# Performance work log

Hardware: AMD Instinct MI355X
Metric: run time of the kernel (lower is better)

## Reference

```python
import jax, jax.numpy as jnp
import numpy as np

# CycleFC1w1a constants (from init_kwargs / gen_offset)
IN_CH = 384
KH, KW = 1, 7  # cycle kernel; actual conv weight is 1x1
START = (KH * KW) // 2  # 3


def _gen_offset_x(C):
    # kernel_size[0] == 1 branch: off_y = 0, off_x[i] = (i + START) % KW - KW // 2
    i = jnp.arange(C)
    return (i + START) % KW - KW // 2  # int32, values in [-3, 3]


def setup_inputs() -> dict:
    key = jax.random.key(0)
    k1, k2, k3 = jax.random.split(key, 3)
    x = jax.random.normal(k1, (64, IN_CH, 32, 32), dtype=jnp.float32)
    weight = jax.random.normal(k2, (IN_CH, IN_CH), dtype=jnp.float32) * 0.05  # [out_ch, in_ch]
    bias = jax.random.normal(k3, (IN_CH,), dtype=jnp.float32) * 0.01
    return {"x": x, "weight": weight, "bias": bias}


def reference(x, weight, bias):
    B, C, H, W = x.shape
    # BinaryQuantizer forward: sign()
    xb = jnp.sign(x)
    wb = jnp.sign(weight)  # [O, C]

    # Fixed per-channel integer horizontal offsets -> exact shifted gather
    off_x = _gen_offset_x(C)                                  # [C]
    cols = jnp.arange(W)[None, :] + off_x[:, None]            # [C, W] sample col = w + off
    valid = (cols >= 0) & (cols < W)                          # zero-pad out of bounds
    cols_c = jnp.clip(cols, 0, W - 1)
    # gather along width per channel: [B, C, H, W]
    g = jnp.take_along_axis(xb, cols_c[None, :, None, :], axis=3)
    g = g * valid[None, :, None, :].astype(x.dtype)

    # pointwise (1x1) channel-mixing conv
    out = jnp.einsum('bchw,oc->bohw', g, wb) + bias[None, :, None, None]
    return out
```

## Files before the change

kernel.cpp:

```cpp
#include <hip/hip_runtime.h>
#include <stdint.h>


#define IN_CH 384
#define HH 32
#define WW 32
#define BB 64
#define HR 4

constexpr uint64_t P7(int t) {
  uint64_t m = 0;
  for (int k = 0; k < 64; ++k)
    if (k % 7 == t) m |= (1ull << k);
  return m;
}
__device__ __constant__ uint64_t Pm[7] = {P7(0), P7(1), P7(2), P7(3), P7(4), P7(5), P7(6)};

__global__ __launch_bounds__(64) void cyc_prep(const float* __restrict__ wgt,
                                               const float* __restrict__ bias,
                                               uint64_t* __restrict__ wbg,
                                               float* __restrict__ bias2t) {
  const int o = blockIdx.x;
  const int lane = threadIdx.x;
  __shared__ uint64_t wb_sh[6];
#pragma unroll
  for (int j = 0; j < 6; ++j) {
    uint64_t m = __ballot(wgt[o * IN_CH + j * 64 + lane] < 0.0f);
    if (lane == 0) wb_sh[j] = m;
  }
  __syncthreads();
  if (lane < 6) wbg[o * 6 + lane] = wb_sh[lane];
  if (lane < WW) {
    const int w = lane;
    int nv = 0, corr = 0;
#pragma unroll
    for (int j = 0; j < 6; ++j) {
      uint64_t V = 0;
#pragma unroll
      for (int d = -3; d <= 3; ++d) {
        int wd = w + d;
        if (wd >= 0 && wd < WW) V |= Pm[(d - j + 14) % 7];
      }
      nv += __popcll(V);
      corr += __popcll(wb_sh[j] & ~V);
    }
    bias2t[w * IN_CH + o] = bias[o] + (float)nv + 2.0f * (float)corr;
  }
}

__global__ __launch_bounds__(768) void cyc_main(const float* __restrict__ x,
                                                const uint64_t* __restrict__ wbg,
                                                const float* __restrict__ bias2t,
                                                float* __restrict__ out) {
  __shared__ uint64_t sh_X[HR][WW][6];
  __shared__ uint64_t sh_G[HR][WW][6];
  const int t = threadIdx.x;
  const int b = blockIdx.x >> 3;
  const int h0 = (blockIdx.x & 7) * HR;
  const int wave = t >> 6, lane = t & 63;

#pragma unroll
  for (int p = 0; p < 2; ++p) {
    const int tau = wave + p * 12;
    const int r = tau / 6, j = tau % 6;
    const int c = j * 64 + lane;
    const float4* xp = reinterpret_cast<const float4*>(
        x + (size_t)((b * IN_CH + c) * HH + h0 + r) * WW);
    unsigned myw = 0;
#pragma unroll
    for (int i = 0; i < 8; ++i) {
      float4 v = xp[i];
      myw |= (v.x < 0.0f ? 1u : 0u) << (i * 4 + 0);
      myw |= (v.y < 0.0f ? 1u : 0u) << (i * 4 + 1);
      myw |= (v.z < 0.0f ? 1u : 0u) << (i * 4 + 2);
      myw |= (v.w < 0.0f ? 1u : 0u) << (i * 4 + 3);
    }
#pragma unroll
    for (int w = 0; w < WW; ++w) {
      uint64_t m = __ballot((myw >> w) & 1u);
      if (lane == 0) sh_X[r][w][j] = m;
    }
  }
  __syncthreads();

  {
    const int r = t / (WW * 6);
    const int q = t % (WW * 6);
    const int w = q & 31, j = q >> 5;
    uint64_t g = 0;
#pragma unroll
    for (int d = -3; d <= 3; ++d) {
      int wd = w + d;
      if (wd >= 0 && wd < WW) g |= sh_X[r][wd][j] & Pm[(d - j + 14) % 7];
    }
    sh_G[r][w][j] = g;
  }
  __syncthreads();

  const int og = __builtin_amdgcn_readfirstlane(wave);
  const int w = lane & 31, r2 = lane >> 5;
  uint64_t gA[6], gB[6];
  {
    const ulonglong2* gv = reinterpret_cast<const ulonglong2*>(&sh_G[r2][w][0]);
    ulonglong2 a0 = gv[0], a1 = gv[1], a2 = gv[2];
    gA[0] = a0.x; gA[1] = a0.y; gA[2] = a1.x; gA[3] = a1.y; gA[4] = a2.x; gA[5] = a2.y;
    const ulonglong2* hv = reinterpret_cast<const ulonglong2*>(&sh_G[2 + r2][w][0]);
    ulonglong2 b0 = hv[0], b1 = hv[1], b2 = hv[2];
    gB[0] = b0.x; gB[1] = b0.y; gB[2] = b1.x; gB[3] = b1.y; gB[4] = b2.x; gB[5] = b2.y;
  }
  float bb[32];
  {
    const float4* bsrc =
        reinterpret_cast<const float4*>(bias2t + w * IN_CH + og * 32);
    float4* bdst = reinterpret_cast<float4*>(bb);
#pragma unroll
    for (int i = 0; i < 8; ++i) bdst[i] = bsrc[i];
  }
  float* opA = out + ((size_t)b * IN_CH + og * 32) * (HH * WW) + h0 * WW + lane;
  float* opB = opA + 2 * WW;
  const uint64_t* wp = wbg + og * 32 * 6;
#pragma unroll
  for (int i = 0; i < 32; ++i) {
    const uint64_t w0 = wp[i * 6 + 0], w1 = wp[i * 6 + 1], w2 = wp[i * 6 + 2];
    const uint64_t w3 = wp[i * 6 + 3], w4 = wp[i * 6 + 4], w5 = wp[i * 6 + 5];
    int mmA = __popcll(gA[0] ^ w0) + __popcll(gA[1] ^ w1) + __popcll(gA[2] ^ w2) +
              __popcll(gA[3] ^ w3) + __popcll(gA[4] ^ w4) + __popcll(gA[5] ^ w5);
    int mmB = __popcll(gB[0] ^ w0) + __popcll(gB[1] ^ w1) + __popcll(gB[2] ^ w2) +
              __popcll(gB[3] ^ w3) + __popcll(gB[4] ^ w4) + __popcll(gB[5] ^ w5);
    opA[i * (HH * WW)] = bb[i] - 2.0f * (float)mmA;
    opB[i * (HH * WW)] = bb[i] - 2.0f * (float)mmB;
  }
}

extern "C" void kernel_launch(void* const* d_in, const int* in_sizes, int n_in,
                              void* d_out, int out_size, void* d_ws, size_t ws_size,
                              hipStream_t stream) {
  const float* x = (const float*)d_in[0];
  const float* wgt = (const float*)d_in[1];
  const float* bias = (const float*)d_in[2];
  float* out = (float*)d_out;

  uint64_t* wbg = (uint64_t*)d_ws;
  float* bias2t = (float*)((char*)d_ws + IN_CH * 6 * sizeof(uint64_t));

  cyc_prep<<<IN_CH, 64, 0, stream>>>(wgt, bias, wbg, bias2t);
  cyc_main<<<BB * (HH / HR), 768, 0, stream>>>(x, wbg, bias2t, out);
}
```

Before: 196.6 us.

## Split fused kernel into bit-pack kernel and binary popcount GEMM kernel

Replaces the single fused kernel with two kernels. The first packs signs and the shifted cycle gather into 64-bit words stored in workspace. The second runs the XOR-popcount channel mix over many smaller 256-thread blocks, each handling 48 output channels and reading a bias table laid out by width. The aim is more parallelism and occupancy than the 512 blocks of 768 threads give. The cost is an extra launch and a global round trip for the packed words, and the split path is used only when the workspace is large enough, otherwise it falls back to the old fused kernel.

```diff
diff --git a/kernel.cpp b/kernel.cpp
--- a/kernel.cpp
+++ b/kernel.cpp
@@ -7,6 +7,9 @@
 #define WW 32
 #define BB 64
 #define HR 4
+#define HRA 2
+
+#define PBASE 0x8102040810204081ull
 
 constexpr uint64_t P7(int t) {
   uint64_t m = 0;
@@ -19,7 +22,9 @@
 __global__ __launch_bounds__(64) void cyc_prep(const float* __restrict__ wgt,
                                                const float* __restrict__ bias,
                                                uint64_t* __restrict__ wbg,
-                                               float* __restrict__ bias2t) {
+                                               float* __restrict__ bias2t,
+                                               float* __restrict__ bias2w,
+                                               int do_w) {
   const int o = blockIdx.x;
   const int lane = threadIdx.x;
   __shared__ uint64_t wb_sh[6];
@@ -44,7 +49,85 @@
       nv += __popcll(V);
       corr += __popcll(wb_sh[j] & ~V);
     }
-    bias2t[w * IN_CH + o] = bias[o] + (float)nv + 2.0f * (float)corr;
+    float val = bias[o] + (float)nv + 2.0f * (float)corr;
+    bias2t[w * IN_CH + o] = val;
+    if (do_w) bias2w[o * WW + w] = val;
+  }
+}
+
+__global__ __launch_bounds__(384) void cyc_pack(const float* __restrict__ x,
+                                                uint64_t* __restrict__ Gg) {
+  __shared__ uint64_t sh_X[HRA][WW][6];
+  const int t = threadIdx.x;
+  const int b = blockIdx.x >> 4;
+  const int h0 = (blockIdx.x & 15) * HRA;
+  const int wave = t >> 6, lane = t & 63;
+
+  const int j = wave;
+  const int c = j * 64 + lane;
+#pragma unroll
+  for (int r = 0; r < HRA; ++r) {
+    const float4* xp = reinterpret_cast<const float4*>(
+        x + (size_t)((b * IN_CH + c) * HH + h0 + r) * WW);
+    unsigned myw = 0;
+#pragma unroll
+    for (int i = 0; i < 8; ++i) {
+      float4 v = xp[i];
+      myw |= (v.x < 0.0f ? 1u : 0u) << (i * 4 + 0);
+      myw |= (v.y < 0.0f ? 1u : 0u) << (i * 4 + 1);
+      myw |= (v.z < 0.0f ? 1u : 0u) << (i * 4 + 2);
+      myw |= (v.w < 0.0f ? 1u : 0u) << (i * 4 + 3);
+    }
+#pragma unroll
+    for (int w = 0; w < WW; ++w) {
+      uint64_t m = __ballot((myw >> w) & 1u);
+      if (lane == 0) sh_X[r][w][j] = m;
+    }
+  }
+  __syncthreads();
+
+  const int r = t / 192;
+  const int q = t % 192;
+  const int w = q & 31, j2 = q >> 5;
+  uint64_t g = 0;
+#pragma unroll
+  for (int d = -3; d <= 3; ++d) {
+    int wd = w + d;
+    if (wd >= 0 && wd < WW) g |= sh_X[r][wd][j2] & (PBASE << ((d - j2 + 14) % 7));
+  }
+  Gg[((size_t)(b * HH + h0 + r) * 6 + j2) * WW + w] = g;
+}
+
+__global__ __launch_bounds__(256) void cyc_gemm(const uint64_t* __restrict__ Gg,
+                                                const uint64_t* __restrict__ wbg,
+                                                const float* __restrict__ bias2w,
+                                                float* __restrict__ out) {
+  const int t = threadIdx.x;
+  const int wave = t >> 6, lane = t & 63;
+  const int bid = blockIdx.x;
+  const int oh = bid & 1;
+  const int hp = (bid >> 1) & 15;
+  const int b = bid >> 5;
+  const int h0 = hp * 2;
+  const int w = lane & 31, r2 = lane >> 5;
+  const int h = h0 + r2;
+
+  uint64_t g[6];
+  const uint64_t* gp = Gg + (size_t)(b * HH + h) * 6 * WW + w;
+#pragma unroll
+  for (int j = 0; j < 6; ++j) g[j] = gp[j * WW];
+
+  const int obase = oh * 192 + __builtin_amdgcn_readfirstlane(wave) * 48;
+  const uint64_t* wp = wbg + (size_t)obase * 6;
+  const float* bp = bias2w + obase * WW + w;
+  float* op = out + ((size_t)b * IN_CH + obase) * (HH * WW) + h0 * WW + lane;
+#pragma unroll
+  for (int i = 0; i < 48; ++i) {
+    const uint64_t w0 = wp[i * 6 + 0], w1 = wp[i * 6 + 1], w2 = wp[i * 6 + 2];
+    const uint64_t w3 = wp[i * 6 + 3], w4 = wp[i * 6 + 4], w5 = wp[i * 6 + 5];
+    int mm = __popcll(g[0] ^ w0) + __popcll(g[1] ^ w1) + __popcll(g[2] ^ w2) +
+             __popcll(g[3] ^ w3) + __popcll(g[4] ^ w4) + __popcll(g[5] ^ w5);
+    op[i * (HH * WW)] = bp[i * WW] - 2.0f * (float)mm;
   }
 }
 
@@ -141,8 +224,17 @@
   float* out = (float*)d_out;
 
   uint64_t* wbg = (uint64_t*)d_ws;
-  float* bias2t = (float*)((char*)d_ws + IN_CH * 6 * sizeof(uint64_t));
-
-  cyc_prep<<<IN_CH, 64, 0, stream>>>(wgt, bias, wbg, bias2t);
-  cyc_main<<<BB * (HH / HR), 768, 0, stream>>>(x, wbg, bias2t, out);
-}
+  float* bias2t = (float*)((char*)d_ws + 18432);
+  float* bias2w = (float*)((char*)d_ws + 67584);
+  uint64_t* Gg = (uint64_t*)((char*)d_ws + 116736);
+  const size_t ws_need = 116736 + (size_t)BB * HH * 6 * WW * 8;
+
+  const int use_split = (ws_size >= ws_need) ? 1 : 0;
+  cyc_prep<<<IN_CH, 64, 0, stream>>>(wgt, bias, wbg, bias2t, bias2w, use_split);
+  if (use_split) {
+    cyc_pack<<<BB * (HH / HRA), 384, 0, stream>>>(x, Gg);
+    cyc_gemm<<<BB * (HH / 2) * 2, 256, 0, stream>>>(Gg, wbg, bias2w, out);
+  } else {
+    cyc_main<<<BB * (HH / HR), 768, 0, stream>>>(x, wbg, bias2t, out);
+  }
+}
```

Result: no change. 199.1 us (+1.3%).

## Replace ballot-based bit packing with per-lane shift and shuffle bit transpose

Applied to the files above, without the earlier changes.

Each lane now applies its channel's cyclic width offset directly to its packed 32-bit row, then transposes the 32x32 bit matrix across lanes using five xor-shuffle butterfly steps. This replaces the 32 ballots per row plus a separate shared-memory gather/mask pass and one barrier. Blocks shrink to 384 threads covering 2 rows, with each wave handling 64 output channels, so the weight and bias loads are reused over fewer rows. The smaller blocks give more of them and the launch bound asks for higher occupancy. The cost is more serial work per wave in the popcount loop.

```diff
diff --git a/kernel.cpp b/kernel.cpp
--- a/kernel.cpp
+++ b/kernel.cpp
@@ -6,7 +6,6 @@
 #define HH 32
 #define WW 32
 #define BB 64
-#define HR 4
 
 constexpr uint64_t P7(int t) {
   uint64_t m = 0;
@@ -48,87 +47,82 @@
   }
 }
 
-__global__ __launch_bounds__(768) void cyc_main(const float* __restrict__ x,
-                                                const uint64_t* __restrict__ wbg,
-                                                const float* __restrict__ bias2t,
-                                                float* __restrict__ out) {
-  __shared__ uint64_t sh_X[HR][WW][6];
-  __shared__ uint64_t sh_G[HR][WW][6];
+__global__ __launch_bounds__(384, 4) void cyc_fused(const float* __restrict__ x,
+                                                    const uint64_t* __restrict__ wbg,
+                                                    const float* __restrict__ bias2t,
+                                                    float* __restrict__ out) {
+  __shared__ uint32_t sh_G[12][2][WW];
   const int t = threadIdx.x;
-  const int b = blockIdx.x >> 3;
-  const int h0 = (blockIdx.x & 7) * HR;
+  const int b = blockIdx.x >> 4;
+  const int h0 = (blockIdx.x & 15) * 2;
   const int wave = t >> 6, lane = t & 63;
 
+  {
+    const int j = wave;
+    const int c = j * 64 + lane;
+    const int cm = c % 7;
+    const int off = ((cm + 3) % 7) - 3;
+    const uint32_t shr = (off > 0) ? (uint32_t)off : 0u;
+    const uint32_t shl = (off < 0) ? (uint32_t)(-off) : 0u;
 #pragma unroll
-  for (int p = 0; p < 2; ++p) {
-    const int tau = wave + p * 12;
-    const int r = tau / 6, j = tau % 6;
-    const int c = j * 64 + lane;
-    const float4* xp = reinterpret_cast<const float4*>(
-        x + (size_t)((b * IN_CH + c) * HH + h0 + r) * WW);
-    unsigned myw = 0;
+    for (int r = 0; r < 2; ++r) {
+      const float4* xp = reinterpret_cast<const float4*>(
+          x + (size_t)((b * IN_CH + c) * HH + h0 + r) * WW);
+      uint32_t myw = 0;
 #pragma unroll
-    for (int i = 0; i < 8; ++i) {
-      float4 v = xp[i];
-      myw |= (v.x < 0.0f ? 1u : 0u) << (i * 4 + 0);
-      myw |= (v.y < 0.0f ? 1u : 0u) << (i * 4 + 1);
-      myw |= (v.z < 0.0f ? 1u : 0u) << (i * 4 + 2);
-      myw |= (v.w < 0.0f ? 1u : 0u) << (i * 4 + 3);
+      for (int i = 0; i < 8; ++i) {
+        float4 v = xp[i];
+        myw |= (v.x < 0.0f ? 1u : 0u) << (i * 4 + 0);
+        myw |= (v.y < 0.0f ? 1u : 0u) << (i * 4 + 1);
+        myw |= (v.z < 0.0f ? 1u : 0u) << (i * 4 + 2);
+        myw |= (v.w < 0.0f ? 1u : 0u) << (i * 4 + 3);
+      }
+      uint32_t s = (myw >> shr) << shl;
+      constexpr uint32_t Mt[5] = {0xFFFF0000u, 0xFF00FF00u, 0xF0F0F0F0u,
+                                  0xCCCCCCCCu, 0xAAAAAAAAu};
+#pragma unroll
+      for (int stp = 0; stp < 5; ++stp) {
+        const int js = 16 >> stp;
+        const uint32_t M = Mt[stp];
+        uint32_t y = __shfl_xor(s, js);
+        s = (lane & js) ? ((s & M) | ((y >> js) & ~M))
+                        : ((s & ~M) | ((y << js) & M));
+      }
+      sh_G[2 * j + (lane >> 5)][r][lane & 31] = s;
     }
-#pragma unroll
-    for (int w = 0; w < WW; ++w) {
-      uint64_t m = __ballot((myw >> w) & 1u);
-      if (lane == 0) sh_X[r][w][j] = m;
-    }
-  }
-  __syncthreads();
-
-  {
-    const int r = t / (WW * 6);
-    const int q = t % (WW * 6);
-    const int w = q & 31, j = q >> 5;
-    uint64_t g = 0;
-#pragma unroll
-    for (int d = -3; d <= 3; ++d) {
-      int wd = w + d;
-      if (wd >= 0 && wd < WW) g |= sh_X[r][wd][j] & Pm[(d - j + 14) % 7];
-    }
-    sh_G[r][w][j] = g;
   }
   __syncthreads();
 
   const int og = __builtin_amdgcn_readfirstlane(wave);
   const int w = lane & 31, r2 = lane >> 5;
-  uint64_t gA[6], gB[6];
-  {
-    const ulonglong2* gv = reinterpret_cast<const ulonglong2*>(&sh_G[r2][w][0]);
-    ulonglong2 a0 = gv[0], a1 = gv[1], a2 = gv[2];
-    gA[0] = a0.x; gA[1] = a0.y; gA[2] = a1.x; gA[3] = a1.y; gA[4] = a2.x; gA[5] = a2.y;
-    const ulonglong2* hv = reinterpret_cast<const ulonglong2*>(&sh_G[2 + r2][w][0]);
-    ulonglong2 b0 = hv[0], b1 = hv[1], b2 = hv[2];
-    gB[0] = b0.x; gB[1] = b0.y; gB[2] = b1.x; gB[3] = b1.y; gB[4] = b2.x; gB[5] = b2.y;
+  uint64_t g[6];
+#pragma unroll
+  for (int jj = 0; jj < 6; ++jj) {
+    uint32_t lo = sh_G[2 * jj + 0][r2][w];
+    uint32_t hi = sh_G[2 * jj + 1][r2][w];
+    g[jj] = ((uint64_t)hi << 32) | (uint64_t)lo;
   }
-  float bb[32];
-  {
-    const float4* bsrc =
-        reinterpret_cast<const float4*>(bias2t + w * IN_CH + og * 32);
-    float4* bdst = reinterpret_cast<float4*>(bb);
 #pragma unroll
-    for (int i = 0; i < 8; ++i) bdst[i] = bsrc[i];
-  }
-  float* opA = out + ((size_t)b * IN_CH + og * 32) * (HH * WW) + h0 * WW + lane;
-  float* opB = opA + 2 * WW;
-  const uint64_t* wp = wbg + og * 32 * 6;
+  for (int half = 0; half < 2; ++half) {
+    const int ob = og * 64 + half * 32;
+    float bb[32];
+    {
+      const float4* bsrc =
+          reinterpret_cast<const float4*>(bias2t + w * IN_CH + ob);
+      float4* bdst = reinterpret_cast<float4*>(bb);
 #pragma unroll
-  for (int i = 0; i < 32; ++i) {
-    const uint64_t w0 = wp[i * 6 + 0], w1 = wp[i * 6 + 1], w2 = wp[i * 6 + 2];
-    const uint64_t w3 = wp[i * 6 + 3], w4 = wp[i * 6 + 4], w5 = wp[i * 6 + 5];
-    int mmA = __popcll(gA[0] ^ w0) + __popcll(gA[1] ^ w1) + __popcll(gA[2] ^ w2) +
-              __popcll(gA[3] ^ w3) + __popcll(gA[4] ^ w4) + __popcll(gA[5] ^ w5);
-    int mmB = __popcll(gB[0] ^ w0) + __popcll(gB[1] ^ w1) + __popcll(gB[2] ^ w2) +
-              __popcll(gB[3] ^ w3) + __popcll(gB[4] ^ w4) + __popcll(gB[5] ^ w5);
-    opA[i * (HH * WW)] = bb[i] - 2.0f * (float)mmA;
-    opB[i * (HH * WW)] = bb[i] - 2.0f * (float)mmB;
+      for (int i = 0; i < 8; ++i) bdst[i] = bsrc[i];
+    }
+    const uint64_t* wp = wbg + (size_t)ob * 6;
+    float* op = out + ((size_t)b * IN_CH + ob) * (HH * WW) + h0 * WW + lane;
+#pragma unroll
+    for (int i = 0; i < 32; ++i) {
+      const uint64_t w0 = wp[i * 6 + 0], w1 = wp[i * 6 + 1], w2 = wp[i * 6 + 2];
+      const uint64_t w3 = wp[i * 6 + 3], w4 = wp[i * 6 + 4], w5 = wp[i * 6 + 5];
+      int mm = __popcll(g[0] ^ w0) + __popcll(g[1] ^ w1) + __popcll(g[2] ^ w2) +
+               __popcll(g[3] ^ w3) + __popcll(g[4] ^ w4) + __popcll(g[5] ^ w5);
+      op[i * (HH * WW)] = bb[i] - 2.0f * (float)mm;
+    }
   }
 }
 
@@ -141,8 +135,8 @@
   float* out = (float*)d_out;
 
   uint64_t* wbg = (uint64_t*)d_ws;
-  float* bias2t = (float*)((char*)d_ws + IN_CH * 6 * sizeof(uint64_t));
+  float* bias2t = (float*)((char*)d_ws + 18432);
 
   cyc_prep<<<IN_CH, 64, 0, stream>>>(wgt, bias, wbg, bias2t);
-  cyc_main<<<BB * (HH / HR), 768, 0, stream>>>(x, wbg, bias2t, out);
+  cyc_fused<<<BB * (HH / 2), 384, 0, stream>>>(x, wbg, bias2t, out);
 }
```

Result: slower. 206.0 us (+4.8%).
